# Kernel optimization log

Measured on AMD Instinct MI355X. Metric: run time of the kernel, lower is better.

Reference implementation:

```python
import jax, jax.numpy as jnp
import numpy as np

B, D_IN, UNITS = 16384, 4096, 4096
EPS = 1e-05

def setup_inputs() -> dict:
    key = jax.random.key(0)
    k1, k2 = jax.random.split(key)
    x = jax.random.normal(k1, (B, D_IN), dtype=jnp.float32)
    # glorot_uniform init for Dense kernel
    limit = np.sqrt(6.0 / (D_IN + UNITS)).astype(np.float32)
    W = jax.random.uniform(k2, (D_IN, UNITS), dtype=jnp.float32, minval=-limit, maxval=limit)
    b = jnp.zeros((UNITS,), dtype=jnp.float32)
    return {"x": x, "W": W, "b": b}

def reference(x, W, b):
    # L2-normalize each row (tf.norm axis=1, keepdims) with +1e-5 stabilizer
    x_norm = jnp.sqrt(jnp.sum(x * x, axis=1, keepdims=True)) + EPS  # [B,1]
    x_dir = x / x_norm                                              # [B,D]
    # dense + bias + ReLU
    return jax.nn.relu(x_dir @ W + b)                               # [B,UNITS]
```

## Files before the change

### kernel.cpp

```cpp
#include <hip/hip_runtime.h>

#define BROWS 16384
#define DIN   4096
#define NOUT  4096
#define EPSV  1e-5f

typedef __attribute__((ext_vector_type(8))) short short8;
typedef __attribute__((ext_vector_type(4))) float f32x4;

__device__ __forceinline__ unsigned short f32_to_bf16(float f) {
    union { float f; unsigned u; } v;
    v.f = f;
    unsigned r = (v.u + 0x7fffu + ((v.u >> 16) & 1u)) >> 16;
    return (unsigned short)r;
}

__global__ __launch_bounds__(256) void normalize_cast_kernel(
    const float* __restrict__ x, unsigned short* __restrict__ A) {
    const int row = blockIdx.x;
    const int tid = threadIdx.x;
    const float4* xr = (const float4*)(x + (size_t)row * DIN);
    float4 v[4];
    float ss = 0.f;
#pragma unroll
    for (int i = 0; i < 4; ++i) {
        v[i] = xr[tid + i * 256];
        ss += v[i].x * v[i].x + v[i].y * v[i].y + v[i].z * v[i].z + v[i].w * v[i].w;
    }
#pragma unroll
    for (int o = 32; o > 0; o >>= 1) ss += __shfl_down(ss, o);
    __shared__ float red[4];
    const int wave = tid >> 6, lane = tid & 63;
    if (lane == 0) red[wave] = ss;
    __syncthreads();
    const float inv = 1.f / (sqrtf(red[0] + red[1] + red[2] + red[3]) + EPSV);
    uint2* Ar = (uint2*)(A + (size_t)row * DIN);
#pragma unroll
    for (int i = 0; i < 4; ++i) {
        uint2 p;
        p.x = (unsigned)f32_to_bf16(v[i].x * inv) | ((unsigned)f32_to_bf16(v[i].y * inv) << 16);
        p.y = (unsigned)f32_to_bf16(v[i].z * inv) | ((unsigned)f32_to_bf16(v[i].w * inv) << 16);
        Ar[tid + i * 256] = p;
    }
}

__global__ __launch_bounds__(256) void transpose_cast_kernel(
    const float* __restrict__ W, unsigned short* __restrict__ Wt) {
    __shared__ float tile[64][65];
    const int bn = blockIdx.x * 64, bk = blockIdx.y * 64;
    const int t = threadIdx.x;
    const int lk = t >> 4, ln4 = (t & 15) * 4;
#pragma unroll
    for (int i = 0; i < 4; ++i) {
        float4 v = *(const float4*)(W + (size_t)(bk + lk + i * 16) * NOUT + bn + ln4);
        tile[lk + i * 16][ln4 + 0] = v.x;
        tile[lk + i * 16][ln4 + 1] = v.y;
        tile[lk + i * 16][ln4 + 2] = v.z;
        tile[lk + i * 16][ln4 + 3] = v.w;
    }
    __syncthreads();
    const int ln = t >> 4, lk4 = (t & 15) * 4;
#pragma unroll
    for (int i = 0; i < 4; ++i) {
        const int n = ln + i * 16;
        uint2 p;
        p.x = (unsigned)f32_to_bf16(tile[lk4 + 0][n]) | ((unsigned)f32_to_bf16(tile[lk4 + 1][n]) << 16);
        p.y = (unsigned)f32_to_bf16(tile[lk4 + 2][n]) | ((unsigned)f32_to_bf16(tile[lk4 + 3][n]) << 16);
        *(uint2*)(Wt + (size_t)(bn + n) * DIN + bk + lk4) = p;
    }
}


__device__ __forceinline__ void async_copy16(const unsigned short* g, unsigned short* l) {
    __builtin_amdgcn_global_load_lds(
        (const __attribute__((address_space(1))) unsigned int*)g,
        (__attribute__((address_space(3))) unsigned int*)l, 16, 0, 0);
}

__global__ __launch_bounds__(256, 2) void gemm_bias_relu_kernel(
    const unsigned short* __restrict__ A, const unsigned short* __restrict__ Wt,
    const float* __restrict__ bias, float* __restrict__ C) {
    __shared__ __align__(16) unsigned short As[128 * 32];
    __shared__ __align__(16) unsigned short Bs[128 * 32];
    const int tid = threadIdx.x;
    const int wave = tid >> 6, lane = tid & 63;
    const int m0 = blockIdx.y * 128, n0 = blockIdx.x * 128;
    const int wr = (wave >> 1) * 64, wc = (wave & 1) * 64;
    const int lm = lane & 15;
    const int q = lane >> 4;
    const int sw = (lm >> 1) & 3;
    const int ksl = (q ^ sw) * 8;

    f32x4 acc[4][4] = {};

    const int c0 = tid, c1 = tid + 256;
    const int p0 = ((c0 & 3) ^ ((c0 >> 3) & 3)) * 8;
    const int p1 = ((c1 & 3) ^ ((c1 >> 3) & 3)) * 8;
    const unsigned short* gA0 = A + (size_t)(m0 + (c0 >> 2)) * DIN + p0;
    const unsigned short* gA1 = A + (size_t)(m0 + (c1 >> 2)) * DIN + p1;
    const unsigned short* gB0 = Wt + (size_t)(n0 + (c0 >> 2)) * DIN + p0;
    const unsigned short* gB1 = Wt + (size_t)(n0 + (c1 >> 2)) * DIN + p1;
    unsigned short* lA0 = &As[(c0 & ~63) * 8];
    unsigned short* lA1 = &As[(c1 & ~63) * 8];
    unsigned short* lB0 = &Bs[(c0 & ~63) * 8];
    unsigned short* lB1 = &Bs[(c1 & ~63) * 8];

    for (int k0 = 0; k0 < DIN; k0 += 32) {
        __syncthreads();
        async_copy16(gA0 + k0, lA0);
        async_copy16(gA1 + k0, lA1);
        async_copy16(gB0 + k0, lB0);
        async_copy16(gB1 + k0, lB1);
        __syncthreads();

        short8 af[4], bf[4];
#pragma unroll
        for (int i = 0; i < 4; ++i)
            af[i] = *(const short8*)(&As[(wr + i * 16 + lm) * 32 + ksl]);
#pragma unroll
        for (int j = 0; j < 4; ++j)
            bf[j] = *(const short8*)(&Bs[(wc + j * 16 + lm) * 32 + ksl]);
#pragma unroll
        for (int i = 0; i < 4; ++i)
#pragma unroll
            for (int j = 0; j < 4; ++j)
                acc[i][j] = __builtin_amdgcn_mfma_f32_16x16x32_bf16(af[i], bf[j], acc[i][j], 0, 0, 0);
    }

    float bj[4];
#pragma unroll
    for (int j = 0; j < 4; ++j) bj[j] = bias[n0 + wc + j * 16 + lm];
    const int colb = n0 + wc + lm;
    const int rowb = m0 + wr + (q << 2);
#pragma unroll
    for (int i = 0; i < 4; ++i) {
#pragma unroll
        for (int r = 0; r < 4; ++r) {
            float* cp = C + (size_t)(rowb + i * 16 + r) * NOUT + colb;
#pragma unroll
            for (int j = 0; j < 4; ++j) {
                float v = acc[i][j][r] + bj[j];
                __builtin_nontemporal_store(v > 0.f ? v : 0.f, cp + j * 16);
            }
        }
    }
}

extern "C" void kernel_launch(void* const* d_in, const int* in_sizes, int n_in,
                              void* d_out, int out_size, void* d_ws, size_t ws_size,
                              hipStream_t stream) {
    const float* x = (const float*)d_in[0];
    const float* W = (const float*)d_in[1];
    const float* b = (const float*)d_in[2];
    float* out = (float*)d_out;

    unsigned short* Abf = (unsigned short*)d_ws;
    unsigned short* Wt = Abf + (size_t)BROWS * DIN;

    normalize_cast_kernel<<<BROWS, 256, 0, stream>>>(x, Abf);
    transpose_cast_kernel<<<dim3(NOUT / 64, DIN / 64), 256, 0, stream>>>(W, Wt);
    gemm_bias_relu_kernel<<<dim3(NOUT / 128, BROWS / 128), 256, 0, stream>>>(Abf, Wt, b, out);
}
```

Measured before the change: 1.092 ms.

## Rewrite GEMM as 256x256 double-buffered pipelined kernel with interleaved async loads

Replaces the 128x128 single-buffer GEMM with a 256x256 tile, K=64 step, 512-thread kernel. Global-to-LDS async copies are double-buffered and interleaved between MFMA phases, gated by s_waitcnt, barriers and setprio. Block IDs are remapped so that neighbouring blocks share tiles in cache. The aim is more reuse per loaded byte and hiding load latency behind matrix math. The cost is 128KB of LDS per block and heavier register pressure, which with launch_bounds(512,2) may limit occupancy or cause spills.

```diff
diff --git a/kernel.cpp b/kernel.cpp
--- a/kernel.cpp
+++ b/kernel.cpp
@@ -4,6 +4,7 @@
 #define DIN   4096
 #define NOUT  4096
 #define EPSV  1e-5f
+#define KT    (DIN / 64)
 
 typedef __attribute__((ext_vector_type(8))) short short8;
 typedef __attribute__((ext_vector_type(4))) float f32x4;
@@ -77,63 +78,134 @@
         (__attribute__((address_space(3))) unsigned int*)l, 16, 0, 0);
 }
 
-__global__ __launch_bounds__(256, 2) void gemm_bias_relu_kernel(
+__global__ __launch_bounds__(512, 2) void gemm_bias_relu_kernel(
     const unsigned short* __restrict__ A, const unsigned short* __restrict__ Wt,
     const float* __restrict__ bias, float* __restrict__ C) {
-    __shared__ __align__(16) unsigned short As[128 * 32];
-    __shared__ __align__(16) unsigned short Bs[128 * 32];
+    __shared__ __align__(16) unsigned short As[2][256 * 64];
+    __shared__ __align__(16) unsigned short Bs[2][256 * 64];
+
     const int tid = threadIdx.x;
-    const int wave = tid >> 6, lane = tid & 63;
-    const int m0 = blockIdx.y * 128, n0 = blockIdx.x * 128;
-    const int wr = (wave >> 1) * 64, wc = (wave & 1) * 64;
-    const int lm = lane & 15;
-    const int q = lane >> 4;
-    const int sw = (lm >> 1) & 3;
-    const int ksl = (q ^ sw) * 8;
-
-    f32x4 acc[4][4] = {};
-
-    const int c0 = tid, c1 = tid + 256;
-    const int p0 = ((c0 & 3) ^ ((c0 >> 3) & 3)) * 8;
-    const int p1 = ((c1 & 3) ^ ((c1 >> 3) & 3)) * 8;
-    const unsigned short* gA0 = A + (size_t)(m0 + (c0 >> 2)) * DIN + p0;
-    const unsigned short* gA1 = A + (size_t)(m0 + (c1 >> 2)) * DIN + p1;
-    const unsigned short* gB0 = Wt + (size_t)(n0 + (c0 >> 2)) * DIN + p0;
-    const unsigned short* gB1 = Wt + (size_t)(n0 + (c1 >> 2)) * DIN + p1;
-    unsigned short* lA0 = &As[(c0 & ~63) * 8];
-    unsigned short* lA1 = &As[(c1 & ~63) * 8];
-    unsigned short* lB0 = &Bs[(c0 & ~63) * 8];
-    unsigned short* lB1 = &Bs[(c1 & ~63) * 8];
-
-    for (int k0 = 0; k0 < DIN; k0 += 32) {
-        __syncthreads();
-        async_copy16(gA0 + k0, lA0);
-        async_copy16(gA1 + k0, lA1);
-        async_copy16(gB0 + k0, lB0);
-        async_copy16(gB1 + k0, lB1);
-        __syncthreads();
-
-        short8 af[4], bf[4];
+    const int lane = tid & 63, wave = tid >> 6;
+    const int wm = wave >> 2, wn = wave & 3;
+    const int lm = lane & 15, q = lane >> 4;
+    const int ko0 = (q ^ (lm >> 1)) * 8;
+    const int ko1 = ko0 ^ 32;
+
+    const int bid = (int)blockIdx.x;
+    const int wg = (bid & 7) * 128 + (bid >> 3);
+    const int n0 = (wg & 15) * 256;
+    const int m0 = (wg >> 4) * 256;
+
+    const int r0 = tid >> 3;
+    const int g0 = (tid & 7) ^ ((r0 & 15) >> 1);
+    const unsigned short* Ag = A + (size_t)(m0 + r0) * DIN + g0 * 8;
+    const unsigned short* Bg = Wt + (size_t)(n0 + r0) * DIN + g0 * 8;
+    const int ub = (tid & ~63) * 8;
+
+#define STG_A(buf, half, kk) do { \
+    const unsigned short* s_ = Ag + (size_t)(half) * (128 * DIN) + (kk); \
+    unsigned short* d_ = &As[buf][(half) * 8192 + ub]; \
+    async_copy16(s_, d_); \
+    async_copy16(s_ + 64 * DIN, d_ + 4096); \
+} while (0)
+#define STG_B(buf, half, kk) do { \
+    const unsigned short* s_ = Bg + (size_t)(half) * (128 * DIN) + (kk); \
+    unsigned short* d_ = &Bs[buf][(half) * 8192 + ub]; \
+    async_copy16(s_, d_); \
+    async_copy16(s_ + 64 * DIN, d_ + 4096); \
+} while (0)
+
+    f32x4 acc[8][4] = {};
+
+    STG_B(0, 0, 0);  STG_B(0, 1, 0);
+    STG_A(0, 0, 0);  STG_A(0, 1, 0);
+    STG_B(1, 0, 64); STG_B(1, 1, 64);
+    STG_A(1, 0, 64);
+    asm volatile("s_waitcnt vmcnt(6)" ::: "memory");
+    __builtin_amdgcn_s_barrier();
+    __builtin_amdgcn_sched_barrier(0);
+
+#pragma unroll 2
+    for (int kt = 0; kt < KT; ++kt) {
+        const int cur = kt & 1;
+        const int kb1 = (kt + 1 < KT ? kt + 1 : KT - 1) * 64;
+        const int kb2 = (kt + 2 < KT ? kt + 2 : KT - 1) * 64;
+        const unsigned short* as = As[cur];
+        const unsigned short* bs = Bs[cur];
+
+        short8 a0[8], a1[8], b0[4], b1[4];
+
+#pragma unroll
+        for (int i = 0; i < 8; ++i)
+            a0[i] = *(const short8*)&as[(wm * 128 + i * 16 + lm) * 64 + ko0];
+#pragma unroll
+        for (int j = 0; j < 4; ++j)
+            b0[j] = *(const short8*)&bs[(wn * 64 + j * 16 + lm) * 64 + ko0];
+        STG_A(cur ^ 1, 1, kb1);
+        __builtin_amdgcn_s_barrier();
+        asm volatile("s_waitcnt lgkmcnt(0)" ::: "memory");
+        __builtin_amdgcn_s_setprio(1);
 #pragma unroll
         for (int i = 0; i < 4; ++i)
-            af[i] = *(const short8*)(&As[(wr + i * 16 + lm) * 32 + ksl]);
+#pragma unroll
+            for (int j = 0; j < 4; ++j)
+                acc[i][j] = __builtin_amdgcn_mfma_f32_16x16x32_bf16(a0[i], b0[j], acc[i][j], 0, 0, 0);
+        __builtin_amdgcn_s_setprio(0);
+        __builtin_amdgcn_s_barrier();
+
 #pragma unroll
         for (int j = 0; j < 4; ++j)
-            bf[j] = *(const short8*)(&Bs[(wc + j * 16 + lm) * 32 + ksl]);
+            b1[j] = *(const short8*)&bs[(wn * 64 + j * 16 + lm) * 64 + ko1];
+        __builtin_amdgcn_s_barrier();
+        asm volatile("s_waitcnt lgkmcnt(0)" ::: "memory");
+        __builtin_amdgcn_s_setprio(1);
+#pragma unroll
+        for (int i = 4; i < 8; ++i)
+#pragma unroll
+            for (int j = 0; j < 4; ++j)
+                acc[i][j] = __builtin_amdgcn_mfma_f32_16x16x32_bf16(a0[i], b0[j], acc[i][j], 0, 0, 0);
+        __builtin_amdgcn_s_setprio(0);
+        __builtin_amdgcn_s_barrier();
+
+#pragma unroll
+        for (int i = 0; i < 8; ++i)
+            a1[i] = *(const short8*)&as[(wm * 128 + i * 16 + lm) * 64 + ko1];
+        STG_B(cur, 0, kb2);
+        STG_B(cur, 1, kb2);
+        __builtin_amdgcn_s_barrier();
+        asm volatile("s_waitcnt lgkmcnt(0)" ::: "memory");
+        __builtin_amdgcn_s_setprio(1);
 #pragma unroll
         for (int i = 0; i < 4; ++i)
 #pragma unroll
             for (int j = 0; j < 4; ++j)
-                acc[i][j] = __builtin_amdgcn_mfma_f32_16x16x32_bf16(af[i], bf[j], acc[i][j], 0, 0, 0);
-    }
+                acc[i][j] = __builtin_amdgcn_mfma_f32_16x16x32_bf16(a1[i], b1[j], acc[i][j], 0, 0, 0);
+        __builtin_amdgcn_s_setprio(0);
+        __builtin_amdgcn_s_barrier();
+
+        STG_A(cur, 0, kb2);
+        asm volatile("s_waitcnt vmcnt(6)" ::: "memory");
+        __builtin_amdgcn_s_barrier();
+        __builtin_amdgcn_s_setprio(1);
+#pragma unroll
+        for (int i = 4; i < 8; ++i)
+#pragma unroll
+            for (int j = 0; j < 4; ++j)
+                acc[i][j] = __builtin_amdgcn_mfma_f32_16x16x32_bf16(a1[i], b1[j], acc[i][j], 0, 0, 0);
+        __builtin_amdgcn_s_setprio(0);
+        __builtin_amdgcn_s_barrier();
+        __builtin_amdgcn_sched_barrier(0);
+    }
+
+    asm volatile("s_waitcnt vmcnt(0)" ::: "memory");
 
     float bj[4];
 #pragma unroll
-    for (int j = 0; j < 4; ++j) bj[j] = bias[n0 + wc + j * 16 + lm];
-    const int colb = n0 + wc + lm;
-    const int rowb = m0 + wr + (q << 2);
-#pragma unroll
-    for (int i = 0; i < 4; ++i) {
+    for (int j = 0; j < 4; ++j) bj[j] = bias[n0 + wn * 64 + j * 16 + lm];
+    const int colb = n0 + wn * 64 + lm;
+    const int rowb = m0 + wm * 128 + (q << 2);
+#pragma unroll
+    for (int i = 0; i < 8; ++i) {
 #pragma unroll
         for (int r = 0; r < 4; ++r) {
             float* cp = C + (size_t)(rowb + i * 16 + r) * NOUT + colb;
@@ -144,6 +216,8 @@
             }
         }
     }
+#undef STG_A
+#undef STG_B
 }
 
 extern "C" void kernel_launch(void* const* d_in, const int* in_sizes, int n_in,
@@ -159,5 +233,5 @@
 
     normalize_cast_kernel<<<BROWS, 256, 0, stream>>>(x, Abf);
     transpose_cast_kernel<<<dim3(NOUT / 64, DIN / 64), 256, 0, stream>>>(W, Wt);
-    gemm_bias_relu_kernel<<<dim3(NOUT / 128, BROWS / 128), 256, 0, stream>>>(Abf, Wt, b, out);
-}
+    gemm_bias_relu_kernel<<<dim3(NOUT / 256 * (BROWS / 256)), 512, 0, stream>>>(Abf, Wt, b, out);
+}
```

After: 1.055 ms. -3.4%, faster.
